# Optimization experiments

Measured on AMD Instinct MI355X. Metric: run time of the kernel, lower is better.

Reference implementation:

```python
import jax, jax.numpy as jnp
import numpy as np

N, E = 4096, 32768
NI, EI, D, EH = 64, 16, 64, 128
NUM_STEPS = 3


def setup_inputs() -> dict:
    key = jax.random.key(0)
    ks = jax.random.split(key, 24)

    def w(k, shape, fan_in):
        return (jax.random.normal(k, shape, jnp.float32) / np.float32(np.sqrt(fan_in)))

    return {
        "node_feats": jax.random.normal(ks[0], (N, NI), jnp.float32),
        "edge_attr": jax.random.normal(ks[1], (E, EI), jnp.float32),
        "edge_index": jax.random.randint(ks[2], (2, E), 0, N),
        # project_node_feats: Linear(NI -> D)
        "W_p": w(ks[3], (NI, D), NI), "b_p": jnp.zeros((D,), jnp.float32),
        # project_edge_feats: Linear(EI -> EH)
        "W_pe": w(ks[4], (EI, EH), EI), "b_pe": jnp.zeros((EH,), jnp.float32),
        # edge_network (NNConv nn): Linear(EH -> D*D)
        "W_nn": w(ks[5], (EH, D * D), EH), "b_nn": jnp.zeros((D * D,), jnp.float32),
        # NNConv root weight + bias
        "W_root": w(ks[6], (D, D), D), "b_conv": jnp.zeros((D,), jnp.float32),
        # GRU (single layer), gate order r, z, n as in torch
        "w_ih": w(ks[7], (D, 3 * D), D), "w_hh": w(ks[8], (D, 3 * D), D),
        "b_ih": jnp.zeros((3 * D,), jnp.float32), "b_hh": jnp.zeros((3 * D,), jnp.float32),
        # edge_update_network: Linear(EH+2D -> EH), Linear(EH -> EH)
        "W_eu1": w(ks[9], (EH + 2 * D, EH), EH + 2 * D), "b_eu1": jnp.zeros((EH,), jnp.float32),
        "W_eu2": w(ks[10], (EH, EH), EH), "b_eu2": jnp.zeros((EH,), jnp.float32),
    }


def reference(node_feats, edge_attr, edge_index, W_p, b_p, W_pe, b_pe,
              W_nn, b_nn, W_root, b_conv, w_ih, w_hh, b_ih, b_hh,
              W_eu1, b_eu1, W_eu2, b_eu2):
    relu = jax.nn.relu
    row, col = edge_index[0], edge_index[1]  # source, target
    n_nodes = node_feats.shape[0]
    d = W_root.shape[0]

    h = relu(node_feats @ W_p + b_p)          # (N, D) projected node feats
    hidden = h                                  # GRU hidden state
    e = relu(edge_attr @ W_pe + b_pe)          # (E, EH) projected edge feats

    for _ in range(NUM_STEPS):
        # NNConv: per-edge weight matrix from edge MLP (dropout=0 in eval)
        We = relu(e @ W_nn + b_nn).reshape(-1, d, d)      # (E, D, D)
        msg = jnp.einsum('ed,edf->ef', h[row], We)        # gather + per-edge matmul
        agg = jax.ops.segment_sum(msg, col, num_segments=n_nodes)  # scatter-add
        m = relu(agg + h @ W_root + b_conv)                # conv output + activation

        # GRU cell (torch gate order: r, z, n)
        gi = m @ w_ih + b_ih
        gh = hidden @ w_hh + b_hh
        ir, iz, i_n = jnp.split(gi, 3, axis=-1)
        hr, hz, h_n = jnp.split(gh, 3, axis=-1)
        r = jax.nn.sigmoid(ir + hr)
        z = jax.nn.sigmoid(iz + hz)
        ncand = jnp.tanh(i_n + r * h_n)
        hidden = (1.0 - z) * ncand + z * hidden
        h = hidden

        # edge update: cat(h[row], h[col], e) -> 2-layer MLP
        ei = jnp.concatenate([h[row], h[col], e], axis=1)
        e = relu(relu(ei @ W_eu1 + b_eu1) @ W_eu2 + b_eu2)

    return h, e
```

## Files before the change

kernel.cpp:

```cpp
#include <hip/hip_runtime.h>
#include <stdint.h>

typedef __attribute__((ext_vector_type(8))) _Float16 f16x8;
typedef __attribute__((ext_vector_type(4))) float f32x4;

#define N_NODES 4096
#define N_EDGES 32768

__device__ __forceinline__ float sigm(float x) { return 1.f / (1.f + __expf(-x)); }

__device__ __forceinline__ f16x8 packh8(const float* p) {
  f16x8 r;
#pragma unroll
  for (int i = 0; i < 8; ++i) r[i] = (_Float16)p[i];
  return r;
}

__global__ void zero_agg_kernel(float* __restrict__ agg) {
  agg[blockIdx.x * 256 + threadIdx.x] = 0.f;
}

__global__ void prep_all(const float* __restrict__ Wnn,
                         const float* __restrict__ We1,
                         const float* __restrict__ We2,
                         _Float16* __restrict__ WnnT,
                         _Float16* __restrict__ We1T,
                         _Float16* __restrict__ We2T) {
  __shared__ float tile[128][33];
  const int b = blockIdx.x, t = threadIdx.x;
  if (b < 128) {
    const int nb = b * 32;
    for (int i = 0; i < 16; ++i) {
      int g = i * 256 + t;
      int k = g >> 5, j = g & 31;
      tile[k][j] = Wnn[(size_t)k * 4096 + nb + j];
    }
    __syncthreads();
    for (int i = 0; i < 16; ++i) {
      int g = i * 256 + t;
      int j = g >> 7, k = g & 127;
      WnnT[(size_t)(nb + j) * 128 + k] = (_Float16)tile[k][j];
    }
  } else {
    int idx = (b - 128) * 256 + t;
    if (idx < 32768) {
      int n = idx >> 8, k = idx & 255;
      We1T[idx] = (_Float16)We1[(size_t)k * 128 + n];
    } else {
      int j = idx - 32768;
      int n = j >> 7, k = j & 127;
      We2T[j] = (_Float16)We2[(size_t)k * 128 + n];
    }
  }
}

__global__ void proj_node_f(const float* __restrict__ nf,
                            const float* __restrict__ Wp,
                            const float* __restrict__ bp,
                            float* __restrict__ h) {
  int idx = blockIdx.x * 256 + threadIdx.x;
  int n = idx >> 6, c = idx & 63;
  float acc = bp[c];
  for (int k = 0; k < 64; ++k)
    acc = fmaf(nf[n * 64 + k], Wp[k * 64 + c], acc);
  h[idx] = fmaxf(acc, 0.f);
}

__launch_bounds__(256)
__global__ void proj_edge_f2(const float* __restrict__ ea,
                             const float* __restrict__ Wpe,
                             const float* __restrict__ bpe,
                             float* __restrict__ e) {
  __shared__ float sw[16 * 128];
  __shared__ float sb[128];
  __shared__ float sa[32][17];
  const int t = threadIdx.x;
  const int ebase = blockIdx.x * 32;
  for (int g = t; g < 2048; g += 256) sw[g] = Wpe[g];
  if (t < 128) sb[t] = bpe[t];
  for (int g = t; g < 512; g += 256) {
    int r = g >> 4, k = g & 15;
    sa[r][k] = ea[(size_t)(ebase + r) * 16 + k];
  }
  __syncthreads();
  int c = t & 127, eg = t >> 7;
  float wc[16];
#pragma unroll
  for (int k = 0; k < 16; ++k) wc[k] = sw[k * 128 + c];
  float bv = sb[c];
#pragma unroll
  for (int i = 0; i < 16; ++i) {
    int ee = eg * 16 + i;
    float acc = bv;
#pragma unroll
    for (int k = 0; k < 16; ++k) acc = fmaf(sa[ee][k], wc[k], acc);
    e[(size_t)(ebase + ee) * 128 + c] = fmaxf(acc, 0.f);
  }
}

__launch_bounds__(512, 1)
__global__ void fused_msg_m(const float* __restrict__ ebf,
                            const float* __restrict__ hid,
                            const _Float16* __restrict__ WnnT,
                            const float* __restrict__ bnn,
                            const int* __restrict__ eidx,
                            float* __restrict__ agg) {
  __shared__ __align__(16) _Float16 Ae[128 * 128];
  __shared__ __align__(16) float Hs[64 * 132];
  const int t = threadIdx.x;
  const int w = t >> 6, l = t & 63, l15 = l & 15, q = l >> 4;
  const int fw = w & 3;
  const int eh = w >> 2;
  const int ebase = blockIdx.x * 128;

#pragma unroll
  for (int i = 0; i < 4; ++i) {
    int g = i * 512 + t;
    int e = g >> 4, d4 = g & 15;
    int r = eidx[ebase + e];
    float4 v = *(const float4*)&hid[(size_t)r * 64 + d4 * 4];
    Hs[(d4 * 4 + 0) * 132 + e] = v.x;
    Hs[(d4 * 4 + 1) * 132 + e] = v.y;
    Hs[(d4 * 4 + 2) * 132 + e] = v.z;
    Hs[(d4 * 4 + 3) * 132 + e] = v.w;
  }
#pragma unroll
  for (int i = 0; i < 4; ++i) {
    int g = i * 512 + t;
    int e = g >> 4, kg = g & 15;
    f16x8 v = packh8(&ebf[(size_t)(ebase + e) * 128 + kg * 8]);
    int kgp = kg ^ (e & 15);
    *(f16x8*)&Ae[e * 128 + kgp * 8] = v;
  }

  float msg[4][4];
#pragma unroll
  for (int m = 0; m < 4; ++m)
#pragma unroll
    for (int rr = 0; rr < 4; ++rr) msg[m][rr] = 0.f;

  __syncthreads();

  const _Float16* wb = WnnT + (size_t)(fw * 16 + l15) * 128 + q * 8;

#pragma unroll 1
  for (int dg = 0; dg < 16; ++dg) {
    f16x8 bb[4][4];
#pragma unroll
    for (int c = 0; c < 4; ++c) {
      const _Float16* p = wb + (size_t)(dg * 4 + c) * 8192;
#pragma unroll
      for (int kk = 0; kk < 4; ++kk) bb[c][kk] = *(const f16x8*)(p + kk * 32);
    }
    float bnv[4];
#pragma unroll
    for (int c = 0; c < 4; ++c) bnv[c] = bnn[(dg * 4 + c) * 64 + fw * 16 + l15];

#pragma unroll
    for (int m = 0; m < 4; ++m) {
      const int arow = (eh * 64 + m * 16 + l15) * 128;
      f32x4 C[4];
#pragma unroll
      for (int c = 0; c < 4; ++c) C[c] = (f32x4){0.f, 0.f, 0.f, 0.f};
#pragma unroll
      for (int kk = 0; kk < 4; ++kk) {
        int kgp = (kk * 4 + q) ^ l15;
        f16x8 a = *(const f16x8*)&Ae[arow + kgp * 8];
#pragma unroll
        for (int c = 0; c < 4; ++c)
          C[c] = __builtin_amdgcn_mfma_f32_16x16x32_f16(a, bb[c][kk], C[c], 0, 0, 0);
      }
#pragma unroll
      for (int c = 0; c < 4; ++c) {
        int d = dg * 4 + c;
        float4 hv = *(const float4*)&Hs[d * 132 + eh * 64 + m * 16 + q * 4];
        msg[m][0] = fmaf(hv.x, fmaxf(C[c][0] + bnv[c], 0.f), msg[m][0]);
        msg[m][1] = fmaf(hv.y, fmaxf(C[c][1] + bnv[c], 0.f), msg[m][1]);
        msg[m][2] = fmaf(hv.z, fmaxf(C[c][2] + bnv[c], 0.f), msg[m][2]);
        msg[m][3] = fmaf(hv.w, fmaxf(C[c][3] + bnv[c], 0.f), msg[m][3]);
      }
    }
    asm volatile("" ::: "memory");
  }

  const int* colp = eidx + N_EDGES;
#pragma unroll
  for (int m = 0; m < 4; ++m)
#pragma unroll
    for (int rr = 0; rr < 4; ++rr) {
      int col = colp[ebase + eh * 64 + m * 16 + q * 4 + rr];
      atomicAdd(&agg[(size_t)col * 64 + fw * 16 + l15], msg[m][rr]);
    }
}

__global__ void node_update_f(const float* __restrict__ agg_r,
                              float* __restrict__ agg_w,
                              float* __restrict__ hid,
                              const float* __restrict__ Wroot,
                              const float* __restrict__ bconv,
                              const float* __restrict__ wih,
                              const float* __restrict__ whh,
                              const float* __restrict__ bih,
                              const float* __restrict__ bhh) {
  __shared__ __align__(16) float sh[16 * 64];
  __shared__ __align__(16) float sm[16 * 64];
  __shared__ __align__(16) float sg[16 * 384];
  const int t = threadIdx.x;
  const int nb = blockIdx.x * 16;

  for (int i = 0; i < 4; ++i) sh[i * 256 + t] = hid[nb * 64 + i * 256 + t];
  __syncthreads();

  for (int i = 0; i < 4; ++i) {
    int idx = i * 256 + t;
    int nl = idx >> 6, dc = idx & 63;
    float acc = bconv[dc] + agg_r[nb * 64 + idx];
    for (int k = 0; k < 64; ++k)
      acc = fmaf(sh[nl * 64 + k], Wroot[k * 64 + dc], acc);
    sm[idx] = fmaxf(acc, 0.f);
  }
  __syncthreads();

  for (int i = 0; i < 24; ++i) {
    int idx = i * 256 + t;
    int nl = idx / 384, j2 = idx % 384;
    float acc;
    if (j2 < 192) {
      acc = bih[j2];
      for (int k = 0; k < 64; ++k)
        acc = fmaf(sm[nl * 64 + k], wih[k * 192 + j2], acc);
    } else {
      int j = j2 - 192;
      acc = bhh[j];
      for (int k = 0; k < 64; ++k)
        acc = fmaf(sh[nl * 64 + k], whh[k * 192 + j], acc);
    }
    sg[idx] = acc;
  }
  __syncthreads();

  for (int i = 0; i < 4; ++i) {
    int idx = i * 256 + t;
    int nl = idx >> 6, dc = idx & 63;
    const float* g = &sg[nl * 384];
    float ir = g[dc], iz = g[64 + dc], in_ = g[128 + dc];
    float hr = g[192 + dc], hz = g[256 + dc], hn = g[320 + dc];
    float r = sigm(ir + hr), z = sigm(iz + hz);
    float nc = tanhf(in_ + r * hn);
    hid[nb * 64 + idx] = (1.f - z) * nc + z * sh[nl * 64 + dc];
    agg_w[nb * 64 + idx] = 0.f;
  }
}

__launch_bounds__(256)
__global__ void edge_mlp_m(const float* __restrict__ hid,
                           float* __restrict__ ebf,
                           const int* __restrict__ eidx,
                           const _Float16* __restrict__ We1T,
                           const float* __restrict__ be1,
                           const _Float16* __restrict__ We2T,
                           const float* __restrict__ be2) {
  __shared__ _Float16 As[64 * 264];
  __shared__ _Float16 Ts[64 * 136];
  const int t = threadIdx.x;
  const int w = t >> 6, l = t & 63, l15 = l & 15, q = l >> 4;
  const int mbase = blockIdx.x * 64;

  for (int g = t; g < 2048; g += 256) {
    int r = g >> 5, kg = g & 31;
    int e = mbase + r;
    const float* src;
    if (kg < 8)       src = &hid[(size_t)eidx[e] * 64 + kg * 8];
    else if (kg < 16) src = &hid[(size_t)eidx[N_EDGES + e] * 64 + (kg - 8) * 8];
    else              src = &ebf[(size_t)e * 128 + (kg - 16) * 8];
    *(f16x8*)&As[r * 264 + kg * 8] = packh8(src);
  }
  __syncthreads();

  f32x4 zero4 = {0.f, 0.f, 0.f, 0.f};
  f32x4 acc[4][2];
#pragma unroll
  for (int m = 0; m < 4; ++m)
#pragma unroll
    for (int nn = 0; nn < 2; ++nn) acc[m][nn] = zero4;

#pragma unroll
  for (int kc = 0; kc < 4; ++kc)
#pragma unroll
    for (int kk = 0; kk < 2; ++kk) {
      int ko = kc * 64 + kk * 32 + q * 8;
      f16x8 b0 = *(const f16x8*)(We1T + (size_t)(w * 32 + l15) * 256 + ko);
      f16x8 b1 = *(const f16x8*)(We1T + (size_t)(w * 32 + 16 + l15) * 256 + ko);
#pragma unroll
      for (int m = 0; m < 4; ++m) {
        f16x8 a = *(const f16x8*)&As[(m * 16 + l15) * 264 + ko];
        acc[m][0] = __builtin_amdgcn_mfma_f32_16x16x32_f16(a, b0, acc[m][0], 0, 0, 0);
        acc[m][1] = __builtin_amdgcn_mfma_f32_16x16x32_f16(a, b1, acc[m][1], 0, 0, 0);
      }
    }

#pragma unroll
  for (int m = 0; m < 4; ++m)
#pragma unroll
    for (int nn = 0; nn < 2; ++nn) {
      int col = w * 32 + nn * 16 + l15;
      float bv = be1[col];
#pragma unroll
      for (int rr = 0; rr < 4; ++rr) {
        int row = m * 16 + q * 4 + rr;
        Ts[row * 136 + col] = (_Float16)fmaxf(acc[m][nn][rr] + bv, 0.f);
      }
    }
  __syncthreads();

  f32x4 acc2[4][2];
#pragma unroll
  for (int m = 0; m < 4; ++m)
#pragma unroll
    for (int nn = 0; nn < 2; ++nn) acc2[m][nn] = zero4;

#pragma unroll
  for (int kc = 0; kc < 2; ++kc)
#pragma unroll
    for (int kk = 0; kk < 2; ++kk) {
      int ko = kc * 64 + kk * 32 + q * 8;
      f16x8 b0 = *(const f16x8*)(We2T + (size_t)(w * 32 + l15) * 128 + ko);
      f16x8 b1 = *(const f16x8*)(We2T + (size_t)(w * 32 + 16 + l15) * 128 + ko);
#pragma unroll
      for (int m = 0; m < 4; ++m) {
        f16x8 a = *(const f16x8*)&Ts[(m * 16 + l15) * 136 + ko];
        acc2[m][0] = __builtin_amdgcn_mfma_f32_16x16x32_f16(a, b0, acc2[m][0], 0, 0, 0);
        acc2[m][1] = __builtin_amdgcn_mfma_f32_16x16x32_f16(a, b1, acc2[m][1], 0, 0, 0);
      }
    }

#pragma unroll
  for (int m = 0; m < 4; ++m)
#pragma unroll
    for (int nn = 0; nn < 2; ++nn) {
      int col = w * 32 + nn * 16 + l15;
      float bv = be2[col];
#pragma unroll
      for (int rr = 0; rr < 4; ++rr) {
        int row = mbase + m * 16 + q * 4 + rr;
        ebf[(size_t)row * 128 + col] = fmaxf(acc2[m][nn][rr] + bv, 0.f);
      }
    }
}

extern "C" void kernel_launch(void* const* d_in, const int* in_sizes, int n_in,
                              void* d_out, int out_size, void* d_ws, size_t ws_size,
                              hipStream_t stream) {
  const float* nf    = (const float*)d_in[0];
  const float* ea    = (const float*)d_in[1];
  const int*   eidx  = (const int*)d_in[2];
  const float* Wp    = (const float*)d_in[3];
  const float* bp    = (const float*)d_in[4];
  const float* Wpe   = (const float*)d_in[5];
  const float* bpe   = (const float*)d_in[6];
  const float* Wnn   = (const float*)d_in[7];
  const float* bnn   = (const float*)d_in[8];
  const float* Wroot = (const float*)d_in[9];
  const float* bconv = (const float*)d_in[10];
  const float* wih   = (const float*)d_in[11];
  const float* whh   = (const float*)d_in[12];
  const float* bih   = (const float*)d_in[13];
  const float* bhh   = (const float*)d_in[14];
  const float* We1   = (const float*)d_in[15];
  const float* be1   = (const float*)d_in[16];
  const float* We2   = (const float*)d_in[17];
  const float* be2   = (const float*)d_in[18];

  float* hid = (float*)d_out;
  float* ebf = (float*)d_out + 4096 * 64;

  char* ws = (char*)d_ws;
  _Float16* WnnT = (_Float16*)(ws + 0);
  _Float16* We1T = (_Float16*)(ws + 1048576);
  _Float16* We2T = (_Float16*)(ws + 1114112);
  float*    agg  = (float*)(ws + 1146880);

  prep_all<<<320, 256, 0, stream>>>(Wnn, We1, We2, WnnT, We1T, We2T);
  proj_node_f<<<1024, 256, 0, stream>>>(nf, Wp, bp, hid);
  proj_edge_f2<<<1024, 256, 0, stream>>>(ea, Wpe, bpe, ebf);
  zero_agg_kernel<<<1024, 256, 0, stream>>>(agg);

  for (int s = 0; s < 3; ++s) {
    fused_msg_m<<<256, 512, 0, stream>>>(ebf, hid, WnnT, bnn, eidx, agg);
    node_update_f<<<256, 256, 0, stream>>>(agg, agg, hid, Wroot, bconv,
                                           wih, whh, bih, bhh);
    edge_mlp_m<<<512, 256, 0, stream>>>(hid, ebf, eidx, We1T, be1, We2T, be2);
  }
}
```

Baseline: 504.4 us.

## Split message kernel into 64-edge by half-D blocks for more occupancy

Restructures the fused NNConv message kernel from 256 blocks of 512 threads (128 edges, all 64 input dims) into 1024 blocks of 256 threads, each handling 64 edges and half of the input dimension d. This shrinks shared memory per block and lets four blocks share a CU, so the grid fills the MI355X's 256 CUs more evenly and hides latency better. The cost is that each edge's fp16 edge features are loaded and converted twice, and twice as many partial messages are atomically added into agg.

```diff
diff --git a/kernel.cpp b/kernel.cpp
--- a/kernel.cpp
+++ b/kernel.cpp
@@ -98,35 +98,36 @@
   }
 }
 
-__launch_bounds__(512, 1)
+__launch_bounds__(256, 4)
 __global__ void fused_msg_m(const float* __restrict__ ebf,
                             const float* __restrict__ hid,
                             const _Float16* __restrict__ WnnT,
                             const float* __restrict__ bnn,
                             const int* __restrict__ eidx,
                             float* __restrict__ agg) {
-  __shared__ __align__(16) _Float16 Ae[128 * 128];
-  __shared__ __align__(16) float Hs[64 * 132];
+  __shared__ __align__(16) _Float16 Ae[64 * 128];
+  __shared__ __align__(16) float Hs[32 * 68];
   const int t = threadIdx.x;
-  const int w = t >> 6, l = t & 63, l15 = l & 15, q = l >> 4;
-  const int fw = w & 3;
-  const int eh = w >> 2;
-  const int ebase = blockIdx.x * 128;
-
+  const int fw = t >> 6, l = t & 63, l15 = l & 15, q = l >> 4;
+  const int eb = blockIdx.x >> 1;
+  const int dh = blockIdx.x & 1;
+  const int ebase = eb * 64;
+  const int dbase = dh * 32;
+
+#pragma unroll
+  for (int i = 0; i < 2; ++i) {
+    int g = i * 256 + t;
+    int e = g >> 3, d4 = g & 7;
+    int r = eidx[ebase + e];
+    float4 v = *(const float4*)&hid[(size_t)r * 64 + dbase + d4 * 4];
+    Hs[(d4 * 4 + 0) * 68 + e] = v.x;
+    Hs[(d4 * 4 + 1) * 68 + e] = v.y;
+    Hs[(d4 * 4 + 2) * 68 + e] = v.z;
+    Hs[(d4 * 4 + 3) * 68 + e] = v.w;
+  }
 #pragma unroll
   for (int i = 0; i < 4; ++i) {
-    int g = i * 512 + t;
-    int e = g >> 4, d4 = g & 15;
-    int r = eidx[ebase + e];
-    float4 v = *(const float4*)&hid[(size_t)r * 64 + d4 * 4];
-    Hs[(d4 * 4 + 0) * 132 + e] = v.x;
-    Hs[(d4 * 4 + 1) * 132 + e] = v.y;
-    Hs[(d4 * 4 + 2) * 132 + e] = v.z;
-    Hs[(d4 * 4 + 3) * 132 + e] = v.w;
-  }
-#pragma unroll
-  for (int i = 0; i < 4; ++i) {
-    int g = i * 512 + t;
+    int g = i * 256 + t;
     int e = g >> 4, kg = g & 15;
     f16x8 v = packh8(&ebf[(size_t)(ebase + e) * 128 + kg * 8]);
     int kgp = kg ^ (e & 15);
@@ -145,35 +146,35 @@
 
 #pragma unroll 1
   for (int dg = 0; dg < 16; ++dg) {
-    f16x8 bb[4][4];
-#pragma unroll
-    for (int c = 0; c < 4; ++c) {
-      const _Float16* p = wb + (size_t)(dg * 4 + c) * 8192;
+    const int d0 = dbase + dg * 2;
+    f16x8 bb[2][4];
+#pragma unroll
+    for (int c = 0; c < 2; ++c) {
+      const _Float16* p = wb + (size_t)(d0 + c) * 8192;
 #pragma unroll
       for (int kk = 0; kk < 4; ++kk) bb[c][kk] = *(const f16x8*)(p + kk * 32);
     }
-    float bnv[4];
-#pragma unroll
-    for (int c = 0; c < 4; ++c) bnv[c] = bnn[(dg * 4 + c) * 64 + fw * 16 + l15];
+    float bnv[2];
+#pragma unroll
+    for (int c = 0; c < 2; ++c) bnv[c] = bnn[(d0 + c) * 64 + fw * 16 + l15];
 
 #pragma unroll
     for (int m = 0; m < 4; ++m) {
-      const int arow = (eh * 64 + m * 16 + l15) * 128;
-      f32x4 C[4];
-#pragma unroll
-      for (int c = 0; c < 4; ++c) C[c] = (f32x4){0.f, 0.f, 0.f, 0.f};
+      const int arow = (m * 16 + l15) * 128;
+      f32x4 C[2];
+      C[0] = (f32x4){0.f, 0.f, 0.f, 0.f};
+      C[1] = (f32x4){0.f, 0.f, 0.f, 0.f};
 #pragma unroll
       for (int kk = 0; kk < 4; ++kk) {
         int kgp = (kk * 4 + q) ^ l15;
         f16x8 a = *(const f16x8*)&Ae[arow + kgp * 8];
-#pragma unroll
-        for (int c = 0; c < 4; ++c)
-          C[c] = __builtin_amdgcn_mfma_f32_16x16x32_f16(a, bb[c][kk], C[c], 0, 0, 0);
-      }
-#pragma unroll
-      for (int c = 0; c < 4; ++c) {
-        int d = dg * 4 + c;
-        float4 hv = *(const float4*)&Hs[d * 132 + eh * 64 + m * 16 + q * 4];
+        C[0] = __builtin_amdgcn_mfma_f32_16x16x32_f16(a, bb[0][kk], C[0], 0, 0, 0);
+        C[1] = __builtin_amdgcn_mfma_f32_16x16x32_f16(a, bb[1][kk], C[1], 0, 0, 0);
+      }
+#pragma unroll
+      for (int c = 0; c < 2; ++c) {
+        int dl = dg * 2 + c;
+        float4 hv = *(const float4*)&Hs[dl * 68 + m * 16 + q * 4];
         msg[m][0] = fmaf(hv.x, fmaxf(C[c][0] + bnv[c], 0.f), msg[m][0]);
         msg[m][1] = fmaf(hv.y, fmaxf(C[c][1] + bnv[c], 0.f), msg[m][1]);
         msg[m][2] = fmaf(hv.z, fmaxf(C[c][2] + bnv[c], 0.f), msg[m][2]);
@@ -188,7 +189,7 @@
   for (int m = 0; m < 4; ++m)
 #pragma unroll
     for (int rr = 0; rr < 4; ++rr) {
-      int col = colp[ebase + eh * 64 + m * 16 + q * 4 + rr];
+      int col = colp[ebase + m * 16 + q * 4 + rr];
       atomicAdd(&agg[(size_t)col * 64 + fw * 16 + l15], msg[m][rr]);
     }
 }
@@ -386,7 +387,7 @@
   zero_agg_kernel<<<1024, 256, 0, stream>>>(agg);
 
   for (int s = 0; s < 3; ++s) {
-    fused_msg_m<<<256, 512, 0, stream>>>(ebf, hid, WnnT, bnn, eidx, agg);
+    fused_msg_m<<<1024, 256, 0, stream>>>(ebf, hid, WnnT, bnn, eidx, agg);
     node_update_f<<<256, 256, 0, stream>>>(agg, agg, hid, Wroot, bconv,
                                            wih, whh, bih, bhh);
     edge_mlp_m<<<512, 256, 0, stream>>>(hid, ebf, eidx, We1T, be1, We2T, be2);
```

Result: slower. 525.1 us (+4.1%).

## Replace atomic scatter-add with CSR gather aggregation and restructure node update

Applied to the files above, without the earlier changes.

Builds a CSR (count, scan, fill) of edges grouped by target node once, then has the message kernel write per-edge fp16 messages to a buffer instead of issuing float atomics into agg. The node update kernel gathers and sums its incoming messages through the CSR, which removes the atomics and the zeroing of agg. The node kernel is also restructured: it stages Wroot in shared memory, keeps transposed h/m tiles, and computes each GRU gate column across 16 nodes in registers. It also rotates the weight-slab order per block in the message loop to spread L2 access. The cost is an extra 4 MB fp16 message buffer round trip, plus extra rounding from storing messages in fp16.

```diff
diff --git a/kernel.cpp b/kernel.cpp
--- a/kernel.cpp
+++ b/kernel.cpp
@@ -14,10 +14,6 @@
 #pragma unroll
   for (int i = 0; i < 8; ++i) r[i] = (_Float16)p[i];
   return r;
-}
-
-__global__ void zero_agg_kernel(float* __restrict__ agg) {
-  agg[blockIdx.x * 256 + threadIdx.x] = 0.f;
 }
 
 __global__ void prep_all(const float* __restrict__ Wnn,
@@ -52,6 +48,41 @@
       We2T[j] = (_Float16)We2[(size_t)k * 128 + n];
     }
   }
+}
+
+__global__ void csr_zero(int* __restrict__ rowcnt) {
+  rowcnt[blockIdx.x * 256 + threadIdx.x] = 0;
+}
+__global__ void csr_count(const int* __restrict__ eidx, int* __restrict__ rowcnt) {
+  int e = blockIdx.x * 256 + threadIdx.x;
+  atomicAdd(&rowcnt[eidx[N_EDGES + e]], 1);
+}
+__global__ void csr_scan(const int* __restrict__ rowcnt,
+                         int* __restrict__ rowptr, int* __restrict__ cursor) {
+  __shared__ int part[1024];
+  const int t = threadIdx.x;
+  const int base = t * 4;
+  int s0 = rowcnt[base], s1 = rowcnt[base + 1], s2 = rowcnt[base + 2], s3 = rowcnt[base + 3];
+  int sum = s0 + s1 + s2 + s3;
+  part[t] = sum;
+  __syncthreads();
+  for (int off = 1; off < 1024; off <<= 1) {
+    int v = (t >= off) ? part[t - off] : 0;
+    __syncthreads();
+    part[t] += v;
+    __syncthreads();
+  }
+  int excl = part[t] - sum;
+  int p0 = excl, p1 = excl + s0, p2 = excl + s0 + s1, p3 = excl + s0 + s1 + s2;
+  rowptr[base] = p0; rowptr[base + 1] = p1; rowptr[base + 2] = p2; rowptr[base + 3] = p3;
+  cursor[base] = p0; cursor[base + 1] = p1; cursor[base + 2] = p2; cursor[base + 3] = p3;
+  if (t == 0) rowptr[4096] = N_EDGES;
+}
+__global__ void csr_fill(const int* __restrict__ eidx, int* __restrict__ cursor,
+                         int* __restrict__ eids) {
+  int e = blockIdx.x * 256 + threadIdx.x;
+  int slot = atomicAdd(&cursor[eidx[N_EDGES + e]], 1);
+  eids[slot] = e;
 }
 
 __global__ void proj_node_f(const float* __restrict__ nf,
@@ -104,7 +135,7 @@
                             const _Float16* __restrict__ WnnT,
                             const float* __restrict__ bnn,
                             const int* __restrict__ eidx,
-                            float* __restrict__ agg) {
+                            _Float16* __restrict__ msgbuf) {
   __shared__ __align__(16) _Float16 Ae[128 * 128];
   __shared__ __align__(16) float Hs[64 * 132];
   const int t = threadIdx.x;
@@ -112,6 +143,7 @@
   const int fw = w & 3;
   const int eh = w >> 2;
   const int ebase = blockIdx.x * 128;
+  const int rot = blockIdx.x & 15;
 
 #pragma unroll
   for (int i = 0; i < 4; ++i) {
@@ -144,17 +176,18 @@
   const _Float16* wb = WnnT + (size_t)(fw * 16 + l15) * 128 + q * 8;
 
 #pragma unroll 1
-  for (int dg = 0; dg < 16; ++dg) {
+  for (int dgi = 0; dgi < 16; ++dgi) {
+    const int dgr = (dgi + rot) & 15;
     f16x8 bb[4][4];
 #pragma unroll
     for (int c = 0; c < 4; ++c) {
-      const _Float16* p = wb + (size_t)(dg * 4 + c) * 8192;
+      const _Float16* p = wb + (size_t)(dgr * 4 + c) * 8192;
 #pragma unroll
       for (int kk = 0; kk < 4; ++kk) bb[c][kk] = *(const f16x8*)(p + kk * 32);
     }
     float bnv[4];
 #pragma unroll
-    for (int c = 0; c < 4; ++c) bnv[c] = bnn[(dg * 4 + c) * 64 + fw * 16 + l15];
+    for (int c = 0; c < 4; ++c) bnv[c] = bnn[(dgr * 4 + c) * 64 + fw * 16 + l15];
 
 #pragma unroll
     for (int m = 0; m < 4; ++m) {
@@ -172,7 +205,7 @@
       }
 #pragma unroll
       for (int c = 0; c < 4; ++c) {
-        int d = dg * 4 + c;
+        int d = dgr * 4 + c;
         float4 hv = *(const float4*)&Hs[d * 132 + eh * 64 + m * 16 + q * 4];
         msg[m][0] = fmaf(hv.x, fmaxf(C[c][0] + bnv[c], 0.f), msg[m][0]);
         msg[m][1] = fmaf(hv.y, fmaxf(C[c][1] + bnv[c], 0.f), msg[m][1]);
@@ -183,18 +216,19 @@
     asm volatile("" ::: "memory");
   }
 
-  const int* colp = eidx + N_EDGES;
 #pragma unroll
   for (int m = 0; m < 4; ++m)
 #pragma unroll
     for (int rr = 0; rr < 4; ++rr) {
-      int col = colp[ebase + eh * 64 + m * 16 + q * 4 + rr];
-      atomicAdd(&agg[(size_t)col * 64 + fw * 16 + l15], msg[m][rr]);
-    }
-}
-
-__global__ void node_update_f(const float* __restrict__ agg_r,
-                              float* __restrict__ agg_w,
+      int e = ebase + eh * 64 + m * 16 + q * 4 + rr;
+      msgbuf[(size_t)e * 64 + fw * 16 + l15] = (_Float16)msg[m][rr];
+    }
+}
+
+__launch_bounds__(256)
+__global__ void node_update_g(const _Float16* __restrict__ msgbuf,
+                              const int* __restrict__ rowptr,
+                              const int* __restrict__ eids,
                               float* __restrict__ hid,
                               const float* __restrict__ Wroot,
                               const float* __restrict__ bconv,
@@ -202,43 +236,74 @@
                               const float* __restrict__ whh,
                               const float* __restrict__ bih,
                               const float* __restrict__ bhh) {
-  __shared__ __align__(16) float sh[16 * 64];
-  __shared__ __align__(16) float sm[16 * 64];
+  __shared__ __align__(16) float shT[64 * 20];
+  __shared__ __align__(16) float smT[64 * 20];
   __shared__ __align__(16) float sg[16 * 384];
+  __shared__ __align__(16) float sW[64 * 64];
   const int t = threadIdx.x;
   const int nb = blockIdx.x * 16;
 
-  for (int i = 0; i < 4; ++i) sh[i * 256 + t] = hid[nb * 64 + i * 256 + t];
-  __syncthreads();
-
+#pragma unroll
+  for (int i = 0; i < 4; ++i) {
+    int g = i * 256 + t;
+    *(float4*)&sW[g * 4] = *(const float4*)&Wroot[g * 4];
+  }
+#pragma unroll
   for (int i = 0; i < 4; ++i) {
     int idx = i * 256 + t;
     int nl = idx >> 6, dc = idx & 63;
-    float acc = bconv[dc] + agg_r[nb * 64 + idx];
+    shT[dc * 20 + nl] = hid[(size_t)(nb + nl) * 64 + dc];
+  }
+  __syncthreads();
+
+#pragma unroll
+  for (int i = 0; i < 4; ++i) {
+    int idx = i * 256 + t;
+    int nl = idx >> 6, dc = idx & 63;
+    int n = nb + nl;
+    float acc = bconv[dc];
+    int r0 = rowptr[n], r1 = rowptr[n + 1];
+    for (int j = r0; j < r1; ++j)
+      acc += (float)msgbuf[(size_t)eids[j] * 64 + dc];
     for (int k = 0; k < 64; ++k)
-      acc = fmaf(sh[nl * 64 + k], Wroot[k * 64 + dc], acc);
-    sm[idx] = fmaxf(acc, 0.f);
-  }
-  __syncthreads();
-
-  for (int i = 0; i < 24; ++i) {
-    int idx = i * 256 + t;
-    int nl = idx / 384, j2 = idx % 384;
-    float acc;
-    if (j2 < 192) {
-      acc = bih[j2];
-      for (int k = 0; k < 64; ++k)
-        acc = fmaf(sm[nl * 64 + k], wih[k * 192 + j2], acc);
-    } else {
-      int j = j2 - 192;
-      acc = bhh[j];
-      for (int k = 0; k < 64; ++k)
-        acc = fmaf(sh[nl * 64 + k], whh[k * 192 + j], acc);
-    }
-    sg[idx] = acc;
-  }
-  __syncthreads();
-
+      acc = fmaf(shT[k * 20 + nl], sW[k * 64 + dc], acc);
+    smT[dc * 20 + nl] = fmaxf(acc, 0.f);
+  }
+  __syncthreads();
+
+  for (int p = 0; p < 2; ++p) {
+    int j2 = p * 256 + t;
+    if (j2 < 384) {
+      bool is_ih = (j2 < 192);
+      int col = is_ih ? j2 : j2 - 192;
+      const float* W = is_ih ? wih : whh;
+      float bias = is_ih ? bih[col] : bhh[col];
+      const float* inT = is_ih ? smT : shT;
+      float a[16];
+#pragma unroll
+      for (int nl = 0; nl < 16; ++nl) a[nl] = bias;
+      for (int k = 0; k < 64; ++k) {
+        float wv = W[k * 192 + col];
+        float4 v0 = *(const float4*)&inT[k * 20 + 0];
+        float4 v1 = *(const float4*)&inT[k * 20 + 4];
+        float4 v2 = *(const float4*)&inT[k * 20 + 8];
+        float4 v3 = *(const float4*)&inT[k * 20 + 12];
+        a[0]  = fmaf(v0.x, wv, a[0]);  a[1]  = fmaf(v0.y, wv, a[1]);
+        a[2]  = fmaf(v0.z, wv, a[2]);  a[3]  = fmaf(v0.w, wv, a[3]);
+        a[4]  = fmaf(v1.x, wv, a[4]);  a[5]  = fmaf(v1.y, wv, a[5]);
+        a[6]  = fmaf(v1.z, wv, a[6]);  a[7]  = fmaf(v1.w, wv, a[7]);
+        a[8]  = fmaf(v2.x, wv, a[8]);  a[9]  = fmaf(v2.y, wv, a[9]);
+        a[10] = fmaf(v2.z, wv, a[10]); a[11] = fmaf(v2.w, wv, a[11]);
+        a[12] = fmaf(v3.x, wv, a[12]); a[13] = fmaf(v3.y, wv, a[13]);
+        a[14] = fmaf(v3.z, wv, a[14]); a[15] = fmaf(v3.w, wv, a[15]);
+      }
+#pragma unroll
+      for (int nl = 0; nl < 16; ++nl) sg[nl * 384 + j2] = a[nl];
+    }
+  }
+  __syncthreads();
+
+#pragma unroll
   for (int i = 0; i < 4; ++i) {
     int idx = i * 256 + t;
     int nl = idx >> 6, dc = idx & 63;
@@ -247,8 +312,7 @@
     float hr = g[192 + dc], hz = g[256 + dc], hn = g[320 + dc];
     float r = sigm(ir + hr), z = sigm(iz + hz);
     float nc = tanhf(in_ + r * hn);
-    hid[nb * 64 + idx] = (1.f - z) * nc + z * sh[nl * 64 + dc];
-    agg_w[nb * 64 + idx] = 0.f;
+    hid[(size_t)nb * 64 + idx] = (1.f - z) * nc + z * shT[dc * 20 + nl];
   }
 }
 
@@ -375,19 +439,26 @@
   float* ebf = (float*)d_out + 4096 * 64;
 
   char* ws = (char*)d_ws;
-  _Float16* WnnT = (_Float16*)(ws + 0);
-  _Float16* We1T = (_Float16*)(ws + 1048576);
-  _Float16* We2T = (_Float16*)(ws + 1114112);
-  float*    agg  = (float*)(ws + 1146880);
+  _Float16* WnnT   = (_Float16*)(ws + 0);
+  _Float16* We1T   = (_Float16*)(ws + 1048576);
+  _Float16* We2T   = (_Float16*)(ws + 1114112);
+  _Float16* msgbuf = (_Float16*)(ws + 1146880);
+  int*      rowptr = (int*)(ws + 5341184);
+  int*      cursor = (int*)(ws + 5357696);
+  int*      eids   = (int*)(ws + 5374080);
 
   prep_all<<<320, 256, 0, stream>>>(Wnn, We1, We2, WnnT, We1T, We2T);
   proj_node_f<<<1024, 256, 0, stream>>>(nf, Wp, bp, hid);
   proj_edge_f2<<<1024, 256, 0, stream>>>(ea, Wpe, bpe, ebf);
-  zero_agg_kernel<<<1024, 256, 0, stream>>>(agg);
+
+  csr_zero<<<16, 256, 0, stream>>>(cursor);
+  csr_count<<<128, 256, 0, stream>>>(eidx, cursor);
+  csr_scan<<<1, 1024, 0, stream>>>(cursor, rowptr, cursor);
+  csr_fill<<<128, 256, 0, stream>>>(eidx, cursor, eids);
 
   for (int s = 0; s < 3; ++s) {
-    fused_msg_m<<<256, 512, 0, stream>>>(ebf, hid, WnnT, bnn, eidx, agg);
-    node_update_f<<<256, 256, 0, stream>>>(agg, agg, hid, Wroot, bconv,
+    fused_msg_m<<<256, 512, 0, stream>>>(ebf, hid, WnnT, bnn, eidx, msgbuf);
+    node_update_g<<<256, 256, 0, stream>>>(msgbuf, rowptr, eids, hid, Wroot, bconv,
                                            wih, whh, bih, bhh);
     edge_mlp_m<<<512, 256, 0, stream>>>(hid, ebf, eidx, We1T, be1, We2T, be2);
   }
```

New measurement: 470.0 us. 6.8% less time.
